# Performance work log

Hardware: AMD Instinct MI355X
Metric: run time of the kernel (lower is better)

Reference implementation:

```python
import jax, jax.numpy as jnp
import numpy as np

PARENTS = np.array([0, 0, 1, 2, 3, 0, 5, 6, 7, 0, 9, 10, 11, 12, 11, 14, 15, 16, 11, 18, 19, 20])
SPARSE_JOINTS = [0, 4, 8, 13, 17, 21]
EE = np.array(SPARSE_JOINTS[1:])                       # end effectors (skip root)
NO_SPARSE = np.array([i for i in range(22) if i not in SPARSE_JOINTS])
LAMBDA_EE = 1.0
LAMBDA_EE_REG = 0.1
IDENT_DQ = np.array([1, 0, 0, 0, 0, 0, 0, 0], dtype=np.float32)


def qmul(a, b):
    # Hamilton product, (w, x, y, z) convention
    aw, ax, ay, az = a[..., 0], a[..., 1], a[..., 2], a[..., 3]
    bw, bx, by, bz = b[..., 0], b[..., 1], b[..., 2], b[..., 3]
    return jnp.stack([
        aw * bw - ax * bx - ay * by - az * bz,
        aw * bx + ax * bw + ay * bz - az * by,
        aw * by - ax * bz + ay * bw + az * bx,
        aw * bz + ax * by - ay * bx + az * bw,
    ], axis=-1)


def qconj(q):
    return q * jnp.array([1.0, -1.0, -1.0, -1.0], dtype=q.dtype)


def quat_to_matrix(q, eps=1e-8):
    # normalize then convert to 3x3 rotation matrix
    q = q / jnp.maximum(jnp.linalg.norm(q, axis=-1, keepdims=True), eps)
    w, x, y, z = q[..., 0], q[..., 1], q[..., 2], q[..., 3]
    m = jnp.stack([
        1 - 2 * (y * y + z * z), 2 * (x * y - w * z), 2 * (x * z + w * y),
        2 * (x * y + w * z), 1 - 2 * (x * x + z * z), 2 * (y * z - w * x),
        2 * (x * z - w * y), 2 * (y * z + w * x), 1 - 2 * (x * x + y * y),
    ], axis=-1)
    return m.reshape(q.shape[:-1] + (3, 3))


def denorm_reshape(d, mean, std, set_root):
    # d: (B, 176, T) -> (B, T, 22, 8)
    d = d * std[None, :, None] + mean[None, :, None]
    if set_root:
        d = d.at[:, :8, :].set(jnp.asarray(IDENT_DQ)[None, :, None])
    B, C, T = d.shape
    return d.reshape(B, C // 8, 8, T).transpose(0, 3, 1, 2)


def local_rots(dq):
    # from_root_dual_quat: local_q[j] = conj(global_q[parent[j]]) * global_q[j]
    # (parents always have lower index than children so the original reversed
    # sequential loop reads untouched parent globals -> fully vectorizable)
    qr = dq[..., :4]                       # (B, T, 22, 4) real part
    loc = qmul(qconj(qr[..., PARENTS, :]), qr)
    # root local rotation forced to identity (as in forward_ik)
    return loc.at[..., 0, :].set(jnp.array([1.0, 0.0, 0.0, 0.0], dtype=dq.dtype))


def fk(local_rot, root_pos, offsets):
    # local_rot: (B, T, J, 4); root_pos: (B, T, 3); offsets: (J, 3)
    mats = quat_to_matrix(local_rot)       # (B, T, J, 3, 3)
    gmats = [mats[..., 0, :, :]]
    gpos = [root_pos]
    for j in range(1, PARENTS.shape[0]):   # fixed 22-joint skeleton walk
        p = int(PARENTS[j])
        gmats.append(jnp.matmul(gmats[p], mats[..., j, :, :]))
        gpos.append(jnp.einsum('btij,j->bti', gmats[p], offsets[j]) + gpos[p])
    return jnp.stack(gpos, axis=2), jnp.stack(gmats, axis=2)


def mse(a, b):
    return jnp.mean(jnp.square(a - b))


def setup_inputs() -> dict:
    key = jax.random.key(0)
    ks = jax.random.split(key, 7)
    B, T, J = 32, 4096, 22
    return {
        'input': jax.random.normal(ks[0], (1, 1), dtype=jnp.float32),
        'input_ik': jax.random.normal(ks[1], (B, (J - 1) * 8, T), dtype=jnp.float32),
        'input_decoder': jax.random.normal(ks[2], (B, J * 8, T), dtype=jnp.float32),
        'target': jax.random.normal(ks[3], (B, J * 8, T), dtype=jnp.float32),
        'mean_dqs': jax.random.normal(ks[4], (J * 8,), dtype=jnp.float32) * 0.1,
        'std_dqs': jax.random.uniform(ks[5], (J * 8,), dtype=jnp.float32, minval=0.5, maxval=1.5),
        'offsets': jax.random.normal(ks[6], (J, 3), dtype=jnp.float32),
    }


def reference(input, input_ik, input_decoder, target, mean_dqs, std_dqs, offsets):
    B, _, T = input_ik.shape
    # pad root dq channels with zeros (then overwritten by identity dq)
    dqs = jnp.concatenate([jnp.zeros((B, 8, T), input_ik.dtype), input_ik], axis=1)
    dqs = denorm_reshape(dqs, mean_dqs, std_dqs, set_root=True)            # (B,T,22,8)
    dqs_dec = denorm_reshape(input_decoder, mean_dqs, std_dqs, set_root=True)
    dqs_tgt = denorm_reshape(target, mean_dqs, std_dqs, set_root=False)

    rot_ik = local_rots(dqs)
    rot_dec = local_rots(dqs_dec)
    rot_tgt = local_rots(dqs_tgt)

    root_pos = jnp.zeros((B, T, 3), dtype=input_ik.dtype)
    pos_ik, mat_ik = fk(rot_ik, root_pos, offsets)
    pos_tgt, mat_tgt = fk(rot_tgt, root_pos, offsets)
    pos_dec, mat_dec = fk(rot_dec, root_pos, offsets)

    loss_ee = mse(pos_ik[:, :, EE, :], pos_tgt[:, :, EE, :])
    loss_ee += mse(mat_ik[:, :, EE, :, :], mat_tgt[:, :, EE, :, :])
    loss_reg = mse(pos_dec[:, :, NO_SPARSE, :], pos_ik[:, :, NO_SPARSE, :])
    loss_reg += mse(mat_dec[:, :, NO_SPARSE, :, :], mat_ik[:, :, NO_SPARSE, :, :])
    return loss_ee * LAMBDA_EE + loss_reg * LAMBDA_EE_REG
```

## Files before the change

kernel.cpp:

```cpp
#include <hip/hip_runtime.h>

#define TDIM 4096
#define SBAR() __builtin_amdgcn_sched_barrier(0)

__device__ __forceinline__ void fk_step(float* __restrict__ f,
                                        const float* __restrict__ q,
                                        float o0, float o1, float o2) {
  const float pw = f[12], px = f[13], py = f[14], pz = f[15];
  float lw = pw*q[0] + px*q[1] + py*q[2] + pz*q[3];
  float lx = pw*q[1] - px*q[0] - py*q[3] + pz*q[2];
  float ly = pw*q[2] + px*q[3] - py*q[0] - pz*q[1];
  float lz = pw*q[3] - px*q[2] + py*q[1] - pz*q[0];
  float n2 = lw*lw + lx*lx + ly*ly + lz*lz;
  float inv = rsqrtf(fmaxf(n2, 1e-16f));
  lw *= inv; lx *= inv; ly *= inv; lz *= inv;
  float xx = lx*lx, yy = ly*ly, zz = lz*lz;
  float xy = lx*ly, xz = lx*lz, yz = ly*lz;
  float wx = lw*lx, wy = lw*ly, wz = lw*lz;
  float m0 = 1.0f-2.0f*(yy+zz), m1 = 2.0f*(xy-wz),      m2 = 2.0f*(xz+wy);
  float m3 = 2.0f*(xy+wz),      m4 = 1.0f-2.0f*(xx+zz), m5 = 2.0f*(yz-wx);
  float m6 = 2.0f*(xz-wy),      m7 = 2.0f*(yz+wx),      m8 = 1.0f-2.0f*(xx+yy);
  f[9]  += f[0]*o0 + f[1]*o1 + f[2]*o2;
  f[10] += f[3]*o0 + f[4]*o1 + f[5]*o2;
  f[11] += f[6]*o0 + f[7]*o1 + f[8]*o2;
  float r0 = f[0]*m0 + f[1]*m3 + f[2]*m6;
  float r1 = f[0]*m1 + f[1]*m4 + f[2]*m7;
  float r2 = f[0]*m2 + f[1]*m5 + f[2]*m8;
  float r3 = f[3]*m0 + f[4]*m3 + f[5]*m6;
  float r4 = f[3]*m1 + f[4]*m4 + f[5]*m7;
  float r5 = f[3]*m2 + f[4]*m5 + f[5]*m8;
  float r6 = f[6]*m0 + f[7]*m3 + f[8]*m6;
  float r7 = f[6]*m1 + f[7]*m4 + f[8]*m7;
  float r8 = f[6]*m2 + f[7]*m5 + f[8]*m8;
  f[0]=r0; f[1]=r1; f[2]=r2; f[3]=r3; f[4]=r4; f[5]=r5; f[6]=r6; f[7]=r7; f[8]=r8;
  f[12]=q[0]; f[13]=q[1]; f[14]=q[2]; f[15]=q[3];
}

__global__ __launch_bounds__(256) void fk_loss_kernel(
    const float* __restrict__ ik,
    const float* __restrict__ dec,
    const float* __restrict__ tgt,
    const float* __restrict__ mean,
    const float* __restrict__ stdv,
    const float* __restrict__ offs,
    float* __restrict__ out)
{
  __shared__ float s_mean[176];
  __shared__ float s_std[176];
  __shared__ float s_wsum[4];
  const int tid = threadIdx.x;
  for (int i = tid; i < 176; i += 256) { s_mean[i] = mean[i]; s_std[i] = stdv[i]; }
  __syncthreads();

  const int idx = blockIdx.x * 256 + tid;
  const int b = idx >> 12;
  const int t = idx & 4095;
  const float* __restrict__ pik  = ik  + ((size_t)b * 168) * TDIM + t;
  const float* __restrict__ pdec = dec + ((size_t)b * 176) * TDIM + t;
  const float* __restrict__ ptgt = tgt + ((size_t)b * 176) * TDIM + t;

  float see_p = 0.f, see_m = 0.f, srg_p = 0.f, srg_m = 0.f;

  float fik[16], fdec[16], ftgt[16];
  float sik[16], sdec[16], stgt[16];
  float rq[4];
  float A[12], B[12], C[12];

#define LOADST(buf, j)                                                         \
  { _Pragma("unroll")                                                          \
    for (int c = 0; c < 4; c++) buf[c]      = pik [(((j)-1)*8 + c) * TDIM];    \
    _Pragma("unroll")                                                          \
    for (int c = 0; c < 4; c++) buf[4 + c]  = pdec[(((j)*8)   + c) * TDIM];    \
    _Pragma("unroll")                                                          \
    for (int c = 0; c < 4; c++) buf[8 + c]  = ptgt[(((j)*8)   + c) * TDIM]; }

#define COMP(buf, j, IS_EE)                                                    \
  { float qi[4], qd[4], qt[4];                                                 \
    _Pragma("unroll")                                                          \
    for (int c = 0; c < 4; c++) {                                              \
      const float sd = s_std[(j)*8 + c], mn = s_mean[(j)*8 + c];               \
      qi[c] = fmaf(buf[c],     sd, mn);                                        \
      qd[c] = fmaf(buf[4+c],   sd, mn);                                        \
      qt[c] = fmaf(buf[8+c],   sd, mn);                                        \
    }                                                                          \
    const float o0 = offs[(j)*3], o1 = offs[(j)*3+1], o2 = offs[(j)*3+2];      \
    fk_step(fik,  qi, o0, o1, o2);                                             \
    fk_step(fdec, qd, o0, o1, o2);                                             \
    fk_step(ftgt, qt, o0, o1, o2);                                             \
    if (IS_EE) {                                                               \
      _Pragma("unroll")                                                        \
      for (int c = 0; c < 3; c++) { float d = fik[9+c] - ftgt[9+c]; see_p = fmaf(d, d, see_p); } \
      _Pragma("unroll")                                                        \
      for (int c = 0; c < 9; c++) { float d = fik[c]   - ftgt[c];   see_m = fmaf(d, d, see_m); } \
    } else {                                                                   \
      _Pragma("unroll")                                                        \
      for (int c = 0; c < 3; c++) { float d = fdec[9+c] - fik[9+c]; srg_p = fmaf(d, d, srg_p); } \
      _Pragma("unroll")                                                        \
      for (int c = 0; c < 9; c++) { float d = fdec[c]   - fik[c];   srg_m = fmaf(d, d, srg_m); } \
    } }

#define RESET()                                                                \
  { _Pragma("unroll")                                                          \
    for (int c = 0; c < 16; c++) { fik[c] = 0.f; fdec[c] = 0.f; ftgt[c] = 0.f; } \
    fik[0]=fik[4]=fik[8]=1.f; fdec[0]=fdec[4]=fdec[8]=1.f; ftgt[0]=ftgt[4]=ftgt[8]=1.f; \
    fik[12]=1.f; fdec[12]=1.f;                                                 \
    ftgt[12]=rq[0]; ftgt[13]=rq[1]; ftgt[14]=rq[2]; ftgt[15]=rq[3]; }

#define SAVE()                                                                 \
  { _Pragma("unroll")                                                          \
    for (int c = 0; c < 16; c++) { sik[c]=fik[c]; sdec[c]=fdec[c]; stgt[c]=ftgt[c]; } }

#define RESTORE()                                                              \
  { _Pragma("unroll")                                                          \
    for (int c = 0; c < 16; c++) { fik[c]=sik[c]; fdec[c]=sdec[c]; ftgt[c]=stgt[c]; } }

  float rqr[4];
  #pragma unroll
  for (int c = 0; c < 4; c++) rqr[c] = ptgt[c * TDIM];
  LOADST(A, 1);
  LOADST(B, 2);
  SBAR();
  #pragma unroll
  for (int c = 0; c < 4; c++) rq[c] = fmaf(rqr[c], s_std[c], s_mean[c]);
  RESET();
  LOADST(C, 3);  COMP(A, 1,  false); SBAR();
  LOADST(A, 4);  COMP(B, 2,  false); SBAR();
  LOADST(B, 5);  COMP(C, 3,  false); SBAR();
  LOADST(C, 6);  COMP(A, 4,  true);  RESET(); SBAR();
  LOADST(A, 7);  COMP(B, 5,  false); SBAR();
  LOADST(B, 8);  COMP(C, 6,  false); SBAR();
  LOADST(C, 9);  COMP(A, 7,  false); SBAR();
  LOADST(A, 10); COMP(B, 8,  true);  RESET(); SBAR();
  LOADST(B, 11); COMP(C, 9,  false); SBAR();
  LOADST(C, 12); COMP(A, 10, false); SBAR();
  LOADST(A, 13); COMP(B, 11, false); SAVE(); SBAR();
  LOADST(B, 14); COMP(C, 12, false); SBAR();
  LOADST(C, 15); COMP(A, 13, true);  RESTORE(); SBAR();
  LOADST(A, 16); COMP(B, 14, false); SBAR();
  LOADST(B, 17); COMP(C, 15, false); SBAR();
  LOADST(C, 18); COMP(A, 16, false); SBAR();
  LOADST(A, 19); COMP(B, 17, true);  RESTORE(); SBAR();
  LOADST(B, 20); COMP(C, 18, false); SBAR();
  LOADST(C, 21); COMP(A, 19, false); SBAR();
  COMP(B, 20, false); SBAR();
  COMP(C, 21, true);

#undef LOADST
#undef COMP
#undef RESET
#undef SAVE
#undef RESTORE

  const float W1 = 1.0f / 1966080.0f;
  const float W2 = 1.0f / 5898240.0f;
  const float W3 = 0.1f / 6291456.0f;
  const float W4 = 0.1f / 18874368.0f;
  float val = see_p * W1 + see_m * W2 + srg_p * W3 + srg_m * W4;

  #pragma unroll
  for (int o = 32; o > 0; o >>= 1) val += __shfl_down(val, o, 64);
  const int wid = tid >> 6, lane = tid & 63;
  if (lane == 0) s_wsum[wid] = val;
  __syncthreads();
  if (tid == 0) atomicAdd(out, s_wsum[0] + s_wsum[1] + s_wsum[2] + s_wsum[3]);
}

extern "C" void kernel_launch(void* const* d_in, const int* in_sizes, int n_in,
                              void* d_out, int out_size, void* d_ws, size_t ws_size,
                              hipStream_t stream) {
  const float* ik   = (const float*)d_in[1];
  const float* dec  = (const float*)d_in[2];
  const float* tgt  = (const float*)d_in[3];
  const float* mean = (const float*)d_in[4];
  const float* stdv = (const float*)d_in[5];
  const float* offs = (const float*)d_in[6];
  float* out = (float*)d_out;

  hipMemsetAsync(out, 0, sizeof(float), stream);
  fk_loss_kernel<<<dim3(512), dim3(256), 0, stream>>>(ik, dec, tgt, mean, stdv, offs, out);
}
```

Baseline: 34.62 us.

## Split three FK chains across warp roles and exchange frames via shared memory

Each block now runs 768 threads in three roles (ik, dec, tgt). Each role runs one forward-kinematics chain instead of one thread running all three. After each joint, the dec or tgt frame is written to double-buffered LDS and the ik role computes the squared-difference losses. The goal is three times the thread-level parallelism and lower register pressure per thread, so the GPU's 256 CUs get more waves. The cost is a __syncthreads per joint (21 barriers), LDS traffic, and ik-role threads doing the loss work while the others idle.

```diff
diff --git a/kernel.cpp b/kernel.cpp
--- a/kernel.cpp
+++ b/kernel.cpp
@@ -36,7 +36,7 @@
   f[12]=q[0]; f[13]=q[1]; f[14]=q[2]; f[15]=q[3];
 }
 
-__global__ __launch_bounds__(256) void fk_loss_kernel(
+__global__ __launch_bounds__(768, 4) void fk_loss_kernel(
     const float* __restrict__ ik,
     const float* __restrict__ dec,
     const float* __restrict__ tgt,
@@ -47,106 +47,106 @@
 {
   __shared__ float s_mean[176];
   __shared__ float s_std[176];
-  __shared__ float s_wsum[4];
+  __shared__ float xbuf[2][12][256];
+  __shared__ float s_wsum[12];
   const int tid = threadIdx.x;
-  for (int i = tid; i < 176; i += 256) { s_mean[i] = mean[i]; s_std[i] = stdv[i]; }
+  for (int i = tid; i < 176; i += 768) { s_mean[i] = mean[i]; s_std[i] = stdv[i]; }
   __syncthreads();
 
-  const int idx = blockIdx.x * 256 + tid;
+  const int role  = tid >> 8;
+  const int inner = tid & 255;
+  const int idx = blockIdx.x * 256 + inner;
   const int b = idx >> 12;
   const int t = idx & 4095;
-  const float* __restrict__ pik  = ik  + ((size_t)b * 168) * TDIM + t;
-  const float* __restrict__ pdec = dec + ((size_t)b * 176) * TDIM + t;
-  const float* __restrict__ ptgt = tgt + ((size_t)b * 176) * TDIM + t;
+
+  const float* __restrict__ p =
+      (role == 0) ? (ik  + ((size_t)b * 168) * TDIM + t - 8 * TDIM)
+    : (role == 1) ? (dec + ((size_t)b * 176) * TDIM + t)
+    :               (tgt + ((size_t)b * 176) * TDIM + t);
 
   float see_p = 0.f, see_m = 0.f, srg_p = 0.f, srg_m = 0.f;
+  float f[16], sv[16], pq[4];
+  float S0[4], S1[4];
 
-  float fik[16], fdec[16], ftgt[16];
-  float sik[16], sdec[16], stgt[16];
-  float rq[4];
-  float A[12], B[12], C[12];
+  pq[0] = 1.f; pq[1] = 0.f; pq[2] = 0.f; pq[3] = 0.f;
+  if (role == 2) {
+    #pragma unroll
+    for (int c = 0; c < 4; c++) pq[c] = fmaf(p[c * TDIM], s_std[c], s_mean[c]);
+  }
 
-#define LOADST(buf, j)                                                         \
+#define LOADJ(buf, j)                                                          \
   { _Pragma("unroll")                                                          \
-    for (int c = 0; c < 4; c++) buf[c]      = pik [(((j)-1)*8 + c) * TDIM];    \
+    for (int c = 0; c < 4; c++) buf[c] = p[((j)*8 + c) * TDIM]; }
+
+#define COMP(buf, j)                                                           \
+  { float q[4];                                                                \
     _Pragma("unroll")                                                          \
-    for (int c = 0; c < 4; c++) buf[4 + c]  = pdec[(((j)*8)   + c) * TDIM];    \
-    _Pragma("unroll")                                                          \
-    for (int c = 0; c < 4; c++) buf[8 + c]  = ptgt[(((j)*8)   + c) * TDIM]; }
+    for (int c = 0; c < 4; c++)                                                \
+      q[c] = fmaf(buf[c], s_std[(j)*8 + c], s_mean[(j)*8 + c]);                \
+    fk_step(f, q, offs[(j)*3], offs[(j)*3 + 1], offs[(j)*3 + 2]); }
 
-#define COMP(buf, j, IS_EE)                                                    \
-  { float qi[4], qd[4], qt[4];                                                 \
-    _Pragma("unroll")                                                          \
-    for (int c = 0; c < 4; c++) {                                              \
-      const float sd = s_std[(j)*8 + c], mn = s_mean[(j)*8 + c];               \
-      qi[c] = fmaf(buf[c],     sd, mn);                                        \
-      qd[c] = fmaf(buf[4+c],   sd, mn);                                        \
-      qt[c] = fmaf(buf[8+c],   sd, mn);                                        \
+#define XCHG(j, IS_EE)                                                         \
+  { if (role == ((IS_EE) ? 2 : 1)) {                                           \
+      _Pragma("unroll")                                                        \
+      for (int c = 0; c < 12; c++) xbuf[(j)&1][c][inner] = f[c];               \
     }                                                                          \
-    const float o0 = offs[(j)*3], o1 = offs[(j)*3+1], o2 = offs[(j)*3+2];      \
-    fk_step(fik,  qi, o0, o1, o2);                                             \
-    fk_step(fdec, qd, o0, o1, o2);                                             \
-    fk_step(ftgt, qt, o0, o1, o2);                                             \
-    if (IS_EE) {                                                               \
-      _Pragma("unroll")                                                        \
-      for (int c = 0; c < 3; c++) { float d = fik[9+c] - ftgt[9+c]; see_p = fmaf(d, d, see_p); } \
-      _Pragma("unroll")                                                        \
-      for (int c = 0; c < 9; c++) { float d = fik[c]   - ftgt[c];   see_m = fmaf(d, d, see_m); } \
-    } else {                                                                   \
-      _Pragma("unroll")                                                        \
-      for (int c = 0; c < 3; c++) { float d = fdec[9+c] - fik[9+c]; srg_p = fmaf(d, d, srg_p); } \
-      _Pragma("unroll")                                                        \
-      for (int c = 0; c < 9; c++) { float d = fdec[c]   - fik[c];   srg_m = fmaf(d, d, srg_m); } \
+    __syncthreads();                                                           \
+    if (role == 0) {                                                           \
+      if (IS_EE) {                                                             \
+        _Pragma("unroll")                                                      \
+        for (int c = 0; c < 3; c++) { float d = f[9+c] - xbuf[(j)&1][9+c][inner]; see_p = fmaf(d, d, see_p); } \
+        _Pragma("unroll")                                                      \
+        for (int c = 0; c < 9; c++) { float d = f[c]   - xbuf[(j)&1][c][inner];   see_m = fmaf(d, d, see_m); } \
+      } else {                                                                 \
+        _Pragma("unroll")                                                      \
+        for (int c = 0; c < 3; c++) { float d = xbuf[(j)&1][9+c][inner] - f[9+c]; srg_p = fmaf(d, d, srg_p); } \
+        _Pragma("unroll")                                                      \
+        for (int c = 0; c < 9; c++) { float d = xbuf[(j)&1][c][inner]   - f[c];   srg_m = fmaf(d, d, srg_m); } \
+      }                                                                        \
     } }
 
 #define RESET()                                                                \
   { _Pragma("unroll")                                                          \
-    for (int c = 0; c < 16; c++) { fik[c] = 0.f; fdec[c] = 0.f; ftgt[c] = 0.f; } \
-    fik[0]=fik[4]=fik[8]=1.f; fdec[0]=fdec[4]=fdec[8]=1.f; ftgt[0]=ftgt[4]=ftgt[8]=1.f; \
-    fik[12]=1.f; fdec[12]=1.f;                                                 \
-    ftgt[12]=rq[0]; ftgt[13]=rq[1]; ftgt[14]=rq[2]; ftgt[15]=rq[3]; }
+    for (int c = 0; c < 16; c++) f[c] = 0.f;                                   \
+    f[0] = f[4] = f[8] = 1.f;                                                  \
+    f[12] = pq[0]; f[13] = pq[1]; f[14] = pq[2]; f[15] = pq[3]; }
 
 #define SAVE()                                                                 \
   { _Pragma("unroll")                                                          \
-    for (int c = 0; c < 16; c++) { sik[c]=fik[c]; sdec[c]=fdec[c]; stgt[c]=ftgt[c]; } }
+    for (int c = 0; c < 16; c++) sv[c] = f[c]; }
 
 #define RESTORE()                                                              \
   { _Pragma("unroll")                                                          \
-    for (int c = 0; c < 16; c++) { fik[c]=sik[c]; fdec[c]=sdec[c]; ftgt[c]=stgt[c]; } }
+    for (int c = 0; c < 16; c++) f[c] = sv[c]; }
 
-  float rqr[4];
-  #pragma unroll
-  for (int c = 0; c < 4; c++) rqr[c] = ptgt[c * TDIM];
-  LOADST(A, 1);
-  LOADST(B, 2);
+  LOADJ(S0, 1);
   SBAR();
-  #pragma unroll
-  for (int c = 0; c < 4; c++) rq[c] = fmaf(rqr[c], s_std[c], s_mean[c]);
   RESET();
-  LOADST(C, 3);  COMP(A, 1,  false); SBAR();
-  LOADST(A, 4);  COMP(B, 2,  false); SBAR();
-  LOADST(B, 5);  COMP(C, 3,  false); SBAR();
-  LOADST(C, 6);  COMP(A, 4,  true);  RESET(); SBAR();
-  LOADST(A, 7);  COMP(B, 5,  false); SBAR();
-  LOADST(B, 8);  COMP(C, 6,  false); SBAR();
-  LOADST(C, 9);  COMP(A, 7,  false); SBAR();
-  LOADST(A, 10); COMP(B, 8,  true);  RESET(); SBAR();
-  LOADST(B, 11); COMP(C, 9,  false); SBAR();
-  LOADST(C, 12); COMP(A, 10, false); SBAR();
-  LOADST(A, 13); COMP(B, 11, false); SAVE(); SBAR();
-  LOADST(B, 14); COMP(C, 12, false); SBAR();
-  LOADST(C, 15); COMP(A, 13, true);  RESTORE(); SBAR();
-  LOADST(A, 16); COMP(B, 14, false); SBAR();
-  LOADST(B, 17); COMP(C, 15, false); SBAR();
-  LOADST(C, 18); COMP(A, 16, false); SBAR();
-  LOADST(A, 19); COMP(B, 17, true);  RESTORE(); SBAR();
-  LOADST(B, 20); COMP(C, 18, false); SBAR();
-  LOADST(C, 21); COMP(A, 19, false); SBAR();
-  COMP(B, 20, false); SBAR();
-  COMP(C, 21, true);
+  LOADJ(S1, 2);  COMP(S0, 1);  XCHG(1, 0);  SBAR();
+  LOADJ(S0, 3);  COMP(S1, 2);  XCHG(2, 0);  SBAR();
+  LOADJ(S1, 4);  COMP(S0, 3);  XCHG(3, 0);  SBAR();
+  LOADJ(S0, 5);  COMP(S1, 4);  XCHG(4, 1);  RESET(); SBAR();
+  LOADJ(S1, 6);  COMP(S0, 5);  XCHG(5, 0);  SBAR();
+  LOADJ(S0, 7);  COMP(S1, 6);  XCHG(6, 0);  SBAR();
+  LOADJ(S1, 8);  COMP(S0, 7);  XCHG(7, 0);  SBAR();
+  LOADJ(S0, 9);  COMP(S1, 8);  XCHG(8, 1);  RESET(); SBAR();
+  LOADJ(S1, 10); COMP(S0, 9);  XCHG(9, 0);  SBAR();
+  LOADJ(S0, 11); COMP(S1, 10); XCHG(10, 0); SBAR();
+  LOADJ(S1, 12); COMP(S0, 11); XCHG(11, 0); SAVE(); SBAR();
+  LOADJ(S0, 13); COMP(S1, 12); XCHG(12, 0); SBAR();
+  LOADJ(S1, 14); COMP(S0, 13); XCHG(13, 1); RESTORE(); SBAR();
+  LOADJ(S0, 15); COMP(S1, 14); XCHG(14, 0); SBAR();
+  LOADJ(S1, 16); COMP(S0, 15); XCHG(15, 0); SBAR();
+  LOADJ(S0, 17); COMP(S1, 16); XCHG(16, 0); SBAR();
+  LOADJ(S1, 18); COMP(S0, 17); XCHG(17, 1); RESTORE(); SBAR();
+  LOADJ(S0, 19); COMP(S1, 18); XCHG(18, 0); SBAR();
+  LOADJ(S1, 20); COMP(S0, 19); XCHG(19, 0); SBAR();
+  LOADJ(S0, 21); COMP(S1, 20); XCHG(20, 0); SBAR();
+  COMP(S0, 21); XCHG(21, 1);
 
-#undef LOADST
+#undef LOADJ
 #undef COMP
+#undef XCHG
 #undef RESET
 #undef SAVE
 #undef RESTORE
@@ -162,7 +162,12 @@
   const int wid = tid >> 6, lane = tid & 63;
   if (lane == 0) s_wsum[wid] = val;
   __syncthreads();
-  if (tid == 0) atomicAdd(out, s_wsum[0] + s_wsum[1] + s_wsum[2] + s_wsum[3]);
+  if (tid == 0) {
+    float s = 0.f;
+    #pragma unroll
+    for (int w = 0; w < 12; w++) s += s_wsum[w];
+    atomicAdd(out, s);
+  }
 }
 
 extern "C" void kernel_launch(void* const* d_in, const int* in_sizes, int n_in,
@@ -177,5 +182,5 @@
   float* out = (float*)d_out;
 
   hipMemsetAsync(out, 0, sizeof(float), stream);
-  fk_loss_kernel<<<dim3(512), dim3(256), 0, stream>>>(ik, dec, tgt, mean, stdv, offs, out);
+  fk_loss_kernel<<<dim3(512), dim3(768), 0, stream>>>(ik, dec, tgt, mean, stdv, offs, out);
 }
```

Result: slower. 49.86 us (+44.0%).

## Stage joint quaternion loads through LDS with async global_load_lds triple buffering

Applied to the files above, without the earlier changes.

Replaces the per-thread register-prefetched strided global loads with 16-byte global_load_lds transfers. Each wavefront copies 3 of the 12 channel rows per joint into a triple-buffered shared tile, and threads then read their own timestep from LDS. Explicit vmcnt waits and a workgroup barrier each round let the next joint's loads overlap the current FK computation. This cuts register pressure and the number of load instructions, but adds a block-wide barrier per joint and more LDS traffic.

```diff
diff --git a/kernel.cpp b/kernel.cpp
--- a/kernel.cpp
+++ b/kernel.cpp
@@ -1,7 +1,17 @@
 #include <hip/hip_runtime.h>
+#include <stdint.h>
 
 #define TDIM 4096
 #define SBAR() __builtin_amdgcn_sched_barrier(0)
+#define WAITV3() asm volatile("s_waitcnt vmcnt(3)" ::: "memory")
+#define WAITV0() asm volatile("s_waitcnt vmcnt(0)" ::: "memory")
+
+__device__ __forceinline__ void gll16(const float* gp, const float* lp) {
+  __builtin_amdgcn_global_load_lds(
+      (const __attribute__((address_space(1))) uint32_t*)(uintptr_t)gp,
+      (__attribute__((address_space(3))) uint32_t*)(uintptr_t)lp,
+      16, 0, 0);
+}
 
 __device__ __forceinline__ void fk_step(float* __restrict__ f,
                                         const float* __restrict__ q,
@@ -47,57 +57,69 @@
 {
   __shared__ float s_mean[176];
   __shared__ float s_std[176];
+  __shared__ float buf[3][12][256];
   __shared__ float s_wsum[4];
   const int tid = threadIdx.x;
   for (int i = tid; i < 176; i += 256) { s_mean[i] = mean[i]; s_std[i] = stdv[i]; }
   __syncthreads();
 
-  const int idx = blockIdx.x * 256 + tid;
-  const int b = idx >> 12;
-  const int t = idx & 4095;
-  const float* __restrict__ pik  = ik  + ((size_t)b * 168) * TDIM + t;
-  const float* __restrict__ pdec = dec + ((size_t)b * 176) * TDIM + t;
-  const float* __restrict__ ptgt = tgt + ((size_t)b * 176) * TDIM + t;
+  const int lane = tid & 63;
+  const int wid  = tid >> 6;
+  const int s0   = wid * 3;
+  const int b  = blockIdx.x >> 4;
+  const int t0 = (blockIdx.x & 15) * 256;
+
+  const float* gpa[3];
+  #pragma unroll
+  for (int k = 0; k < 3; k++) {
+    const int s = s0 + k;
+    const float* q;
+    if (s < 4)      q = ik  + (size_t)b * 168 * TDIM + (size_t)s       * TDIM;
+    else if (s < 8) q = dec + (size_t)b * 176 * TDIM + (size_t)(s + 4) * TDIM;
+    else            q = tgt + (size_t)b * 176 * TDIM + (size_t)s       * TDIM;
+    gpa[k] = q + t0 + lane * 4;
+  }
+
+  const float* tp = tgt + (size_t)b * 176 * TDIM + t0 + tid;
+  float rq[4];
+  #pragma unroll
+  for (int c = 0; c < 4; c++) rq[c] = fmaf(tp[c * TDIM], s_std[c], s_mean[c]);
 
   float see_p = 0.f, see_m = 0.f, srg_p = 0.f, srg_m = 0.f;
-
   float fik[16], fdec[16], ftgt[16];
   float sik[16], sdec[16], stgt[16];
-  float rq[4];
-  float A[12], B[12], C[12];
-
-#define LOADST(buf, j)                                                         \
-  { _Pragma("unroll")                                                          \
-    for (int c = 0; c < 4; c++) buf[c]      = pik [(((j)-1)*8 + c) * TDIM];    \
-    _Pragma("unroll")                                                          \
-    for (int c = 0; c < 4; c++) buf[4 + c]  = pdec[(((j)*8)   + c) * TDIM];    \
-    _Pragma("unroll")                                                          \
-    for (int c = 0; c < 4; c++) buf[8 + c]  = ptgt[(((j)*8)   + c) * TDIM]; }
-
-#define COMP(buf, j, IS_EE)                                                    \
+
+#define ISSUE(P)                                                               \
+  { gll16(gpa[0], &buf[P][s0 + 0][0]);                                         \
+    gll16(gpa[1], &buf[P][s0 + 1][0]);                                         \
+    gll16(gpa[2], &buf[P][s0 + 2][0]);                                         \
+    gpa[0] += 8 * TDIM; gpa[1] += 8 * TDIM; gpa[2] += 8 * TDIM; }
+
+#define COMPJ(P, j)                                                            \
   { float qi[4], qd[4], qt[4];                                                 \
     _Pragma("unroll")                                                          \
     for (int c = 0; c < 4; c++) {                                              \
       const float sd = s_std[(j)*8 + c], mn = s_mean[(j)*8 + c];               \
-      qi[c] = fmaf(buf[c],     sd, mn);                                        \
-      qd[c] = fmaf(buf[4+c],   sd, mn);                                        \
-      qt[c] = fmaf(buf[8+c],   sd, mn);                                        \
+      qi[c] = fmaf(buf[P][c][tid],     sd, mn);                                \
+      qd[c] = fmaf(buf[P][4 + c][tid], sd, mn);                                \
+      qt[c] = fmaf(buf[P][8 + c][tid], sd, mn);                                \
     }                                                                          \
     const float o0 = offs[(j)*3], o1 = offs[(j)*3+1], o2 = offs[(j)*3+2];      \
     fk_step(fik,  qi, o0, o1, o2);                                             \
     fk_step(fdec, qd, o0, o1, o2);                                             \
-    fk_step(ftgt, qt, o0, o1, o2);                                             \
-    if (IS_EE) {                                                               \
-      _Pragma("unroll")                                                        \
-      for (int c = 0; c < 3; c++) { float d = fik[9+c] - ftgt[9+c]; see_p = fmaf(d, d, see_p); } \
-      _Pragma("unroll")                                                        \
-      for (int c = 0; c < 9; c++) { float d = fik[c]   - ftgt[c];   see_m = fmaf(d, d, see_m); } \
-    } else {                                                                   \
-      _Pragma("unroll")                                                        \
-      for (int c = 0; c < 3; c++) { float d = fdec[9+c] - fik[9+c]; srg_p = fmaf(d, d, srg_p); } \
-      _Pragma("unroll")                                                        \
-      for (int c = 0; c < 9; c++) { float d = fdec[c]   - fik[c];   srg_m = fmaf(d, d, srg_m); } \
-    } }
+    fk_step(ftgt, qt, o0, o1, o2); }
+
+#define DIFF_EE()                                                              \
+  { _Pragma("unroll")                                                          \
+    for (int c = 0; c < 3; c++) { float d = fik[9+c] - ftgt[9+c]; see_p = fmaf(d, d, see_p); } \
+    _Pragma("unroll")                                                          \
+    for (int c = 0; c < 9; c++) { float d = fik[c]   - ftgt[c];   see_m = fmaf(d, d, see_m); } }
+
+#define DIFF_NS()                                                              \
+  { _Pragma("unroll")                                                          \
+    for (int c = 0; c < 3; c++) { float d = fdec[9+c] - fik[9+c]; srg_p = fmaf(d, d, srg_p); } \
+    _Pragma("unroll")                                                          \
+    for (int c = 0; c < 9; c++) { float d = fdec[c]   - fik[c];   srg_m = fmaf(d, d, srg_m); } }
 
 #define RESET()                                                                \
   { _Pragma("unroll")                                                          \
@@ -112,44 +134,48 @@
 
 #define RESTORE()                                                              \
   { _Pragma("unroll")                                                          \
-    for (int c = 0; c < 16; c++) { fik[c]=sik[c]; fdec[c]=sdec[c]; ftgt[c]=stgt[c]; } }
-
-  float rqr[4];
-  #pragma unroll
-  for (int c = 0; c < 4; c++) rqr[c] = ptgt[c * TDIM];
-  LOADST(A, 1);
-  LOADST(B, 2);
-  SBAR();
-  #pragma unroll
-  for (int c = 0; c < 4; c++) rq[c] = fmaf(rqr[c], s_std[c], s_mean[c]);
+    for (int c = 0; c < 16; c++) { fik[c]=sik[c]; fdec[c]=sdec[c]; stgt[c]; ftgt[c]=stgt[c]; } }
+
+#define ROUND(r)                                                               \
+  ISSUE((r) % 3); SBAR(); WAITV3();                                            \
+  __builtin_amdgcn_s_barrier(); SBAR();                                        \
+  COMPJ((((r) - 1) % 3), r);
+
+  ISSUE(0);
   RESET();
-  LOADST(C, 3);  COMP(A, 1,  false); SBAR();
-  LOADST(A, 4);  COMP(B, 2,  false); SBAR();
-  LOADST(B, 5);  COMP(C, 3,  false); SBAR();
-  LOADST(C, 6);  COMP(A, 4,  true);  RESET(); SBAR();
-  LOADST(A, 7);  COMP(B, 5,  false); SBAR();
-  LOADST(B, 8);  COMP(C, 6,  false); SBAR();
-  LOADST(C, 9);  COMP(A, 7,  false); SBAR();
-  LOADST(A, 10); COMP(B, 8,  true);  RESET(); SBAR();
-  LOADST(B, 11); COMP(C, 9,  false); SBAR();
-  LOADST(C, 12); COMP(A, 10, false); SBAR();
-  LOADST(A, 13); COMP(B, 11, false); SAVE(); SBAR();
-  LOADST(B, 14); COMP(C, 12, false); SBAR();
-  LOADST(C, 15); COMP(A, 13, true);  RESTORE(); SBAR();
-  LOADST(A, 16); COMP(B, 14, false); SBAR();
-  LOADST(B, 17); COMP(C, 15, false); SBAR();
-  LOADST(C, 18); COMP(A, 16, false); SBAR();
-  LOADST(A, 19); COMP(B, 17, true);  RESTORE(); SBAR();
-  LOADST(B, 20); COMP(C, 18, false); SBAR();
-  LOADST(C, 21); COMP(A, 19, false); SBAR();
-  COMP(B, 20, false); SBAR();
-  COMP(C, 21, true);
-
-#undef LOADST
-#undef COMP
+
+  ROUND(1);  DIFF_NS();
+  ROUND(2);  DIFF_NS();
+  ROUND(3);  DIFF_NS();
+  ROUND(4);  DIFF_EE(); RESET();
+  ROUND(5);  DIFF_NS();
+  ROUND(6);  DIFF_NS();
+  ROUND(7);  DIFF_NS();
+  ROUND(8);  DIFF_EE(); RESET();
+  ROUND(9);  DIFF_NS();
+  ROUND(10); DIFF_NS();
+  ROUND(11); DIFF_NS(); SAVE();
+  ROUND(12); DIFF_NS();
+  ROUND(13); DIFF_EE(); RESTORE();
+  ROUND(14); DIFF_NS();
+  ROUND(15); DIFF_NS();
+  ROUND(16); DIFF_NS();
+  ROUND(17); DIFF_EE(); RESTORE();
+  ROUND(18); DIFF_NS();
+  ROUND(19); DIFF_NS();
+  ROUND(20); DIFF_NS();
+  SBAR(); WAITV0();
+  __builtin_amdgcn_s_barrier(); SBAR();
+  COMPJ(2, 21); DIFF_EE();
+
+#undef ISSUE
+#undef COMPJ
+#undef DIFF_EE
+#undef DIFF_NS
 #undef RESET
 #undef SAVE
 #undef RESTORE
+#undef ROUND
 
   const float W1 = 1.0f / 1966080.0f;
   const float W2 = 1.0f / 5898240.0f;
@@ -159,7 +185,6 @@
 
   #pragma unroll
   for (int o = 32; o > 0; o >>= 1) val += __shfl_down(val, o, 64);
-  const int wid = tid >> 6, lane = tid & 63;
   if (lane == 0) s_wsum[wid] = val;
   __syncthreads();
   if (tid == 0) atomicAdd(out, s_wsum[0] + s_wsum[1] + s_wsum[2] + s_wsum[3]);
```

Result: slower. 35.42 us (+2.3%).

## Split skeleton chains across four block roles driven by a slot table

Applied to the files above, without the earlier changes.

Each time step is now handled by four blocks, each walking a subset of kinematic chains from a constant slot table, instead of one thread walking all 21 joints. The shared prefix joints (9-11) are recomputed by the three blocks that need them. This quadruples the grid to raise parallelism and latency hiding on a 512-block launch. In exchange it replaces the fully unrolled, software-pipelined load schedule with a runtime loop that does dependent table loads, adds redundant FK work and extra global reads, and quadruples the atomics.

```diff
diff --git a/kernel.cpp b/kernel.cpp
--- a/kernel.cpp
+++ b/kernel.cpp
@@ -1,7 +1,20 @@
 #include <hip/hip_runtime.h>
 
 #define TDIM 4096
-#define SBAR() __builtin_amdgcn_sched_barrier(0)
+
+typedef struct { int ik_ch, dq_ch, off3, flags; } Slot;
+
+__device__ const Slot g_slots[4][8] = {
+  { {  0,  8,  3, 1}, {  8, 16,  6, 1}, { 16, 24,  9, 1}, { 24, 32, 12, 6},
+    { 32, 40, 15, 1}, { 40, 48, 18, 1}, { 48, 56, 21, 1}, { 56, 64, 24, 2} },
+  { { 64, 72, 27, 1}, { 72, 80, 30, 1}, { 80, 88, 33, 1}, { 88, 96, 36, 1},
+    { 96,104, 39, 2}, {  0,  0,  0, 0}, {  0,  0,  0, 0}, {  0,  0,  0, 0} },
+  { { 64, 72, 27, 0}, { 72, 80, 30, 0}, { 80, 88, 33, 0}, {104,112, 42, 1},
+    {112,120, 45, 1}, {120,128, 48, 1}, {128,136, 51, 2}, {  0,  0,  0, 0} },
+  { { 64, 72, 27, 0}, { 72, 80, 30, 0}, { 80, 88, 33, 0}, {136,144, 54, 1},
+    {144,152, 57, 1}, {152,160, 60, 1}, {160,168, 63, 2}, {  0,  0,  0, 0} },
+};
+__device__ const int g_nslots[4] = { 8, 5, 7, 7 };
 
 __device__ __forceinline__ void fk_step(float* __restrict__ f,
                                         const float* __restrict__ q,
@@ -52,52 +65,20 @@
   for (int i = tid; i < 176; i += 256) { s_mean[i] = mean[i]; s_std[i] = stdv[i]; }
   __syncthreads();
 
-  const int idx = blockIdx.x * 256 + tid;
+  const int role = blockIdx.x & 3;
+  const int idx  = (blockIdx.x >> 2) * 256 + tid;
   const int b = idx >> 12;
   const int t = idx & 4095;
-  const float* __restrict__ pik  = ik  + ((size_t)b * 168) * TDIM + t;
-  const float* __restrict__ pdec = dec + ((size_t)b * 176) * TDIM + t;
-  const float* __restrict__ ptgt = tgt + ((size_t)b * 176) * TDIM + t;
+  const float* __restrict__ pik  = ik  + (size_t)b * 168 * TDIM + t;
+  const float* __restrict__ pdec = dec + (size_t)b * 176 * TDIM + t;
+  const float* __restrict__ ptgt = tgt + (size_t)b * 176 * TDIM + t;
+
+  float rq[4];
+  #pragma unroll
+  for (int c = 0; c < 4; c++) rq[c] = fmaf(ptgt[c * TDIM], s_std[c], s_mean[c]);
 
   float see_p = 0.f, see_m = 0.f, srg_p = 0.f, srg_m = 0.f;
-
   float fik[16], fdec[16], ftgt[16];
-  float sik[16], sdec[16], stgt[16];
-  float rq[4];
-  float A[12], B[12], C[12];
-
-#define LOADST(buf, j)                                                         \
-  { _Pragma("unroll")                                                          \
-    for (int c = 0; c < 4; c++) buf[c]      = pik [(((j)-1)*8 + c) * TDIM];    \
-    _Pragma("unroll")                                                          \
-    for (int c = 0; c < 4; c++) buf[4 + c]  = pdec[(((j)*8)   + c) * TDIM];    \
-    _Pragma("unroll")                                                          \
-    for (int c = 0; c < 4; c++) buf[8 + c]  = ptgt[(((j)*8)   + c) * TDIM]; }
-
-#define COMP(buf, j, IS_EE)                                                    \
-  { float qi[4], qd[4], qt[4];                                                 \
-    _Pragma("unroll")                                                          \
-    for (int c = 0; c < 4; c++) {                                              \
-      const float sd = s_std[(j)*8 + c], mn = s_mean[(j)*8 + c];               \
-      qi[c] = fmaf(buf[c],     sd, mn);                                        \
-      qd[c] = fmaf(buf[4+c],   sd, mn);                                        \
-      qt[c] = fmaf(buf[8+c],   sd, mn);                                        \
-    }                                                                          \
-    const float o0 = offs[(j)*3], o1 = offs[(j)*3+1], o2 = offs[(j)*3+2];      \
-    fk_step(fik,  qi, o0, o1, o2);                                             \
-    fk_step(fdec, qd, o0, o1, o2);                                             \
-    fk_step(ftgt, qt, o0, o1, o2);                                             \
-    if (IS_EE) {                                                               \
-      _Pragma("unroll")                                                        \
-      for (int c = 0; c < 3; c++) { float d = fik[9+c] - ftgt[9+c]; see_p = fmaf(d, d, see_p); } \
-      _Pragma("unroll")                                                        \
-      for (int c = 0; c < 9; c++) { float d = fik[c]   - ftgt[c];   see_m = fmaf(d, d, see_m); } \
-    } else {                                                                   \
-      _Pragma("unroll")                                                        \
-      for (int c = 0; c < 3; c++) { float d = fdec[9+c] - fik[9+c]; srg_p = fmaf(d, d, srg_p); } \
-      _Pragma("unroll")                                                        \
-      for (int c = 0; c < 9; c++) { float d = fdec[c]   - fik[c];   srg_m = fmaf(d, d, srg_m); } \
-    } }
 
 #define RESET()                                                                \
   { _Pragma("unroll")                                                          \
@@ -106,50 +87,51 @@
     fik[12]=1.f; fdec[12]=1.f;                                                 \
     ftgt[12]=rq[0]; ftgt[13]=rq[1]; ftgt[14]=rq[2]; ftgt[15]=rq[3]; }
 
-#define SAVE()                                                                 \
-  { _Pragma("unroll")                                                          \
-    for (int c = 0; c < 16; c++) { sik[c]=fik[c]; sdec[c]=fdec[c]; stgt[c]=ftgt[c]; } }
+  RESET();
 
-#define RESTORE()                                                              \
-  { _Pragma("unroll")                                                          \
-    for (int c = 0; c < 16; c++) { fik[c]=sik[c]; fdec[c]=sdec[c]; ftgt[c]=stgt[c]; } }
+  const int nslots = g_nslots[role];
+  #pragma unroll 1
+  for (int k = 0; k < nslots; ++k) {
+    const int ikch  = g_slots[role][k].ik_ch;
+    const int dqch  = g_slots[role][k].dq_ch;
+    const int off3  = g_slots[role][k].off3;
+    const int flags = g_slots[role][k].flags;
 
-  float rqr[4];
-  #pragma unroll
-  for (int c = 0; c < 4; c++) rqr[c] = ptgt[c * TDIM];
-  LOADST(A, 1);
-  LOADST(B, 2);
-  SBAR();
-  #pragma unroll
-  for (int c = 0; c < 4; c++) rq[c] = fmaf(rqr[c], s_std[c], s_mean[c]);
-  RESET();
-  LOADST(C, 3);  COMP(A, 1,  false); SBAR();
-  LOADST(A, 4);  COMP(B, 2,  false); SBAR();
-  LOADST(B, 5);  COMP(C, 3,  false); SBAR();
-  LOADST(C, 6);  COMP(A, 4,  true);  RESET(); SBAR();
-  LOADST(A, 7);  COMP(B, 5,  false); SBAR();
-  LOADST(B, 8);  COMP(C, 6,  false); SBAR();
-  LOADST(C, 9);  COMP(A, 7,  false); SBAR();
-  LOADST(A, 10); COMP(B, 8,  true);  RESET(); SBAR();
-  LOADST(B, 11); COMP(C, 9,  false); SBAR();
-  LOADST(C, 12); COMP(A, 10, false); SBAR();
-  LOADST(A, 13); COMP(B, 11, false); SAVE(); SBAR();
-  LOADST(B, 14); COMP(C, 12, false); SBAR();
-  LOADST(C, 15); COMP(A, 13, true);  RESTORE(); SBAR();
-  LOADST(A, 16); COMP(B, 14, false); SBAR();
-  LOADST(B, 17); COMP(C, 15, false); SBAR();
-  LOADST(C, 18); COMP(A, 16, false); SBAR();
-  LOADST(A, 19); COMP(B, 17, true);  RESTORE(); SBAR();
-  LOADST(B, 20); COMP(C, 18, false); SBAR();
-  LOADST(C, 21); COMP(A, 19, false); SBAR();
-  COMP(B, 20, false); SBAR();
-  COMP(C, 21, true);
+    float qi[4], qd[4], qt[4];
+    #pragma unroll
+    for (int c = 0; c < 4; c++) {
+      qi[c] = pik [(size_t)(ikch + c) * TDIM];
+      qd[c] = pdec[(size_t)(dqch + c) * TDIM];
+      qt[c] = ptgt[(size_t)(dqch + c) * TDIM];
+    }
+    #pragma unroll
+    for (int c = 0; c < 4; c++) {
+      const float sd = s_std[dqch + c], mn = s_mean[dqch + c];
+      qi[c] = fmaf(qi[c], sd, mn);
+      qd[c] = fmaf(qd[c], sd, mn);
+      qt[c] = fmaf(qt[c], sd, mn);
+    }
+    const float o0 = offs[off3], o1 = offs[off3 + 1], o2 = offs[off3 + 2];
+    fk_step(fik,  qi, o0, o1, o2);
+    fk_step(fdec, qd, o0, o1, o2);
+    fk_step(ftgt, qt, o0, o1, o2);
 
-#undef LOADST
-#undef COMP
+    if (flags & 1) {
+      #pragma unroll
+      for (int c = 0; c < 3; c++) { float d = fdec[9+c] - fik[9+c]; srg_p = fmaf(d, d, srg_p); }
+      #pragma unroll
+      for (int c = 0; c < 9; c++) { float d = fdec[c]   - fik[c];   srg_m = fmaf(d, d, srg_m); }
+    }
+    if (flags & 2) {
+      #pragma unroll
+      for (int c = 0; c < 3; c++) { float d = fik[9+c] - ftgt[9+c]; see_p = fmaf(d, d, see_p); }
+      #pragma unroll
+      for (int c = 0; c < 9; c++) { float d = fik[c]   - ftgt[c];   see_m = fmaf(d, d, see_m); }
+    }
+    if (flags & 4) RESET();
+  }
+
 #undef RESET
-#undef SAVE
-#undef RESTORE
 
   const float W1 = 1.0f / 1966080.0f;
   const float W2 = 1.0f / 5898240.0f;
@@ -159,8 +141,8 @@
 
   #pragma unroll
   for (int o = 32; o > 0; o >>= 1) val += __shfl_down(val, o, 64);
-  const int wid = tid >> 6, lane = tid & 63;
-  if (lane == 0) s_wsum[wid] = val;
+  const int wid = tid >> 6;
+  if ((tid & 63) == 0) s_wsum[wid] = val;
   __syncthreads();
   if (tid == 0) atomicAdd(out, s_wsum[0] + s_wsum[1] + s_wsum[2] + s_wsum[3]);
 }
@@ -177,5 +159,5 @@
   float* out = (float*)d_out;
 
   hipMemsetAsync(out, 0, sizeof(float), stream);
-  fk_loss_kernel<<<dim3(512), dim3(256), 0, stream>>>(ik, dec, tgt, mean, stdv, offs, out);
+  fk_loss_kernel<<<dim3(2048), dim3(256), 0, stream>>>(ik, dec, tgt, mean, stdv, offs, out);
 }
```

New measurement: 64.07 us. +85.1%, slower.
